# Performance work log

Hardware: AMD Instinct MI355X
Metric: run time of the kernel (lower is better)

The kernel has to match this reference:

```python
import jax, jax.numpy as jnp
import numpy as np

WS = 8          # window_size
SHIFT = 4       # shift_size
HEADS = 8
HD = 32         # head_dim
DIM = 256       # embedding_dim
PWS = 8         # pretrained_window_size
EPS = 1e-5


def _rel_tables():
    # log-spaced relative coords table, shape ((2*WS-1)^2, 2)
    r = np.arange(-(WS - 1), WS, dtype=np.float32)
    tb = np.stack(np.meshgrid(r, r, indexing='ij'), 0).reshape(2, -1).T
    tb = tb / (PWS - 1) * 8.0
    tb = np.sign(tb) * np.log2(np.abs(tb) + 1.0) / np.log2(8.0)
    # relative position index, shape (m, m)
    ch = np.arange(WS)
    coords = np.stack(np.meshgrid(ch, ch, indexing='ij'), 0).reshape(2, -1)
    rel = (coords[:, :, None] - coords[:, None, :]).transpose(1, 2, 0).astype(np.int64)
    rel[..., 0] += WS - 1
    rel[..., 1] += WS - 1
    rel[..., 0] *= 2 * WS - 1
    return tb.astype(np.float32), rel.sum(-1)


def _shift_mask(h, w):
    # standard Swin SW-MSA mask: region labels -> -100 where regions differ
    img = np.zeros((h, w), np.int32)
    cnt = 0
    for hs in (slice(0, h - WS), slice(h - WS, h - SHIFT), slice(h - SHIFT, h)):
        for wsl in (slice(0, w - WS), slice(w - WS, w - SHIFT), slice(w - SHIFT, w)):
            img[hs, wsl] = cnt
            cnt += 1
    nh, nw = h // WS, w // WS
    m = WS * WS
    mw = img.reshape(nh, WS, nw, WS).transpose(0, 2, 1, 3).reshape(nh * nw, m)
    return np.where(mw[:, None, :] != mw[:, :, None], -100.0, 0.0).astype(np.float32)


def _ln(x, g, b):
    mu = x.mean(-1, keepdims=True)
    var = ((x - mu) ** 2).mean(-1, keepdims=True)
    return (x - mu) * jax.lax.rsqrt(var + EPS) * g + b


def setup_inputs() -> dict:
    key = jax.random.key(0)
    ks = jax.random.split(key, 8)
    s = 0.02
    return {
        'x': jax.random.normal(ks[0], (2, DIM, 256, 256), jnp.float32),
        'qkv_w': jax.random.normal(ks[1], (DIM, 3 * HEADS * HD), jnp.float32) * s,
        'logit_scale': jnp.full((HEADS,), np.log(10.0), jnp.float32),
        'proj_w': jax.random.normal(ks[2], (HEADS * HD, DIM), jnp.float32) * s,
        'proj_b': jnp.zeros((DIM,), jnp.float32),
        'ln1_w': jnp.ones((DIM,), jnp.float32),
        'ln1_b': jnp.zeros((DIM,), jnp.float32),
        'fc1_w': jax.random.normal(ks[3], (DIM, 4 * DIM), jnp.float32) * s,
        'fc1_b': jnp.zeros((4 * DIM,), jnp.float32),
        'fc2_w': jax.random.normal(ks[4], (4 * DIM, DIM), jnp.float32) * s,
        'fc2_b': jnp.zeros((DIM,), jnp.float32),
        'ln2_w': jnp.ones((DIM,), jnp.float32),
        'ln2_b': jnp.zeros((DIM,), jnp.float32),
        'cpb_w1': jax.random.normal(ks[5], (2, 512), jnp.float32) * s,
        'cpb_b1': jnp.zeros((512,), jnp.float32),
        'cpb_w2': jax.random.normal(ks[6], (512, HEADS), jnp.float32) * s,
    }


def reference(x, qkv_w, logit_scale, proj_w, proj_b, ln1_w, ln1_b,
              fc1_w, fc1_b, fc2_w, fc2_b, ln2_w, ln2_b,
              cpb_w1, cpb_b1, cpb_w2):
    b, c, h, w = x.shape
    nh, nw = h // WS, w // WS
    Nw, m = nh * nw, WS * WS
    tb_np, idx_np = _rel_tables()
    smask = jnp.asarray(_shift_mask(h, w))              # (Nw, m, m)

    # cyclic shift
    xs = jnp.roll(x, (-SHIFT, -SHIFT), axis=(2, 3))

    # relative position bias via MLP, then 16*sigmoid
    bt = jax.nn.relu(jnp.asarray(tb_np) @ cpb_w1 + cpb_b1) @ cpb_w2   # (T, H)
    rpe = bt[jnp.asarray(idx_np).reshape(-1)].reshape(m, m, HEADS)
    bias = 16.0 * jax.nn.sigmoid(rpe.transpose(2, 0, 1))              # (H, m, m)
    amask = bias[None] + smask[:, None]                               # (Nw, H, m, m)

    # window partition: (b, c, h, w) -> (b, Nw, m, c)
    xw = xs.reshape(b, c, nh, WS, nw, WS).transpose(0, 2, 4, 3, 5, 1).reshape(b, Nw, m, c)

    # cosine attention
    qkv = (xw @ qkv_w).reshape(b, Nw, m, 3, HEADS, HD).transpose(3, 0, 1, 4, 2, 5)
    q, k, v = qkv[0], qkv[1], qkv[2]                                  # (b, Nw, H, m, HD)
    qn = q / jnp.maximum(jnp.linalg.norm(q, axis=-1, keepdims=True), 1e-12)
    kn = k / jnp.maximum(jnp.linalg.norm(k, axis=-1, keepdims=True), 1e-12)
    scale = jnp.exp(jnp.minimum(logit_scale, np.log(100.0)))          # (H,)
    logits = jnp.einsum('bnhid,bnhjd->bnhij', qn, kn) * scale[None, None, :, None, None]
    logits = logits + amask[None]
    p = jax.nn.softmax(logits, axis=-1)
    o = jnp.einsum('bnhij,bnhjd->bnhid', p, v)
    o = o.transpose(0, 1, 3, 2, 4).reshape(b, Nw, m, HEADS * HD) @ proj_w + proj_b

    # post-norm residuals
    y = _ln(o, ln1_w, ln1_b) + xw
    mlp = jax.nn.gelu(y @ fc1_w + fc1_b, approximate=False) @ fc2_w + fc2_b
    y = _ln(mlp, ln2_w, ln2_b) + y

    # window reverse + un-shift
    xr = y.reshape(b, nh, nw, WS, WS, c).transpose(0, 5, 1, 3, 2, 4).reshape(b, c, h, w)
    return jnp.roll(xr, (SHIFT, SHIFT), axis=(2, 3))
```

## Files before the change

### kernel.cpp

```cpp
#include <hip/hip_runtime.h>
#include <hip/hip_bf16.h>

typedef __attribute__((ext_vector_type(4))) float f32x4;
typedef __attribute__((ext_vector_type(8))) short s16x8;
typedef __attribute__((ext_vector_type(4))) unsigned short u16x4;

#define L_XW   0
#define L_SLAB 32768
#define L_NQ   131072
#define L_NK   133120
#define L_Y    131072
#define L_H0   0
#define L_H1   32768
#define L_H2   65536
#define L_H3   98304
#define L_MB   0
#define SMEM_BYTES 163840

#define WSO_BIAS   0
#define WSO_QKVW   131072
#define WSO_PROJW  524288
#define WSO_FC1W   655360
#define WSO_FC2W   1179648
#define WSO_SIN    1703936ULL
#define WSO_SOUT   68812800ULL

#define LOG2E 1.4426950408f

__device__ __forceinline__ unsigned short f2bf(float f) {
  __hip_bfloat16 h = __float2bfloat16(f);
  return __builtin_bit_cast(unsigned short, h);
}
__device__ __forceinline__ float bf2f(unsigned short b) {
  union { unsigned u; float f; } v; v.u = ((unsigned)b) << 16;
  return v.f;
}
__device__ __forceinline__ int swzb(int row, int byteoff) {
  return byteoff ^ ((row & 7) << 4);
}

__global__ __launch_bounds__(256)
void prep_kernel(const float* __restrict__ qkv_w,
                 const float* __restrict__ proj_w,
                 const float* __restrict__ fc1_w,
                 const float* __restrict__ fc2_w,
                 const float* __restrict__ cpb_w1,
                 const float* __restrict__ cpb_b1,
                 const float* __restrict__ cpb_w2,
                 const float* __restrict__ x,
                 const float* __restrict__ ls,
                 unsigned char* __restrict__ wsb) {
  __shared__ float tile[64][66];
  const int bid = blockIdx.x;
  const int tid = threadIdx.x;

  if (bid < 3072) {
    int e = bid * 256 + tid;
    const float* src; unsigned short* dst; int K, N; int eo; bool perm;
    if (e < 196608)       { eo = e;          src = qkv_w;  dst = (unsigned short*)(wsb + WSO_QKVW);  K = 256;  N = 768;  perm = false; }
    else if (e < 262144)  { eo = e - 196608; src = proj_w; dst = (unsigned short*)(wsb + WSO_PROJW); K = 256;  N = 256;  perm = true; }
    else if (e < 524288)  { eo = e - 262144; src = fc1_w;  dst = (unsigned short*)(wsb + WSO_FC1W);  K = 256;  N = 1024; perm = false; }
    else                  { eo = e - 524288; src = fc2_w;  dst = (unsigned short*)(wsb + WSO_FC2W);  K = 1024; N = 256;  perm = true; }
    int j = eo & 7, c = (eo >> 3) & 15, rest = eo >> 7;
    int Kg = K >> 3;
    int kg = rest % Kg, nt = rest / Kg;
    int s = kg * 8 + j;
    if (perm) s = (s & ~31) | ((s & 1) << 4) | ((s & 31) >> 1);
    dst[eo] = f2bf(src[s * N + nt * 16 + c]);
  } else if (bid == 3072) {
    float (*bt)[8] = (float(*)[8])&tile[0][0];
    for (int t = tid; t < 225; t += 256) {
      int a = t / 15, b = t % 15;
      float r0 = (float)(a - 7) * (8.0f / 7.0f);
      float r1 = (float)(b - 7) * (8.0f / 7.0f);
      float f0 = (r0 >= 0.f ? 1.f : -1.f) * log2f(fabsf(r0) + 1.f) * (1.f / 3.f);
      float f1 = (r1 >= 0.f ? 1.f : -1.f) * log2f(fabsf(r1) + 1.f) * (1.f / 3.f);
      float acc[8] = {0.f,0.f,0.f,0.f,0.f,0.f,0.f,0.f};
      for (int k = 0; k < 512; ++k) {
        float hv = f0 * cpb_w1[k] + f1 * cpb_w1[512 + k] + cpb_b1[k];
        hv = fmaxf(hv, 0.f);
        #pragma unroll
        for (int h = 0; h < 8; ++h) acc[h] += hv * cpb_w2[k * 8 + h];
      }
      #pragma unroll
      for (int h = 0; h < 8; ++h) bt[t][h] = acc[h];
    }
    __syncthreads();
    float* biasp = (float*)(wsb + WSO_BIAS);
    for (int e = tid; e < 32768; e += 256) {
      int nn = e & 3, cc = (e >> 2) & 15, i = (e >> 6) & 63, h = e >> 12;
      int j = nn * 16 + cc;
      int dr = (i >> 3) - (j >> 3) + 7, dc = (i & 7) - (j & 7) + 7;
      float v = bt[dr * 15 + dc][h];
      float scale = __expf(fminf(ls[h], 4.6051702f));
      biasp[e] = LOG2E * (16.f / (1.f + expf(-v)) - (scale + 16.f));
    }
  } else {
    int b2 = bid - 3073;
    int pb = b2 & 1023;
    int cg = (b2 >> 10) & 3;
    int b  = b2 >> 12;
    int p0 = pb * 64, c0 = cg * 64;
    unsigned short* sg = (unsigned short*)(wsb + WSO_SIN);

    int pi = tid & 63, cq = tid >> 6;
    for (int r = 0; r < 16; ++r) {
      int c = cq * 16 + r;
      tile[pi][c] = x[((size_t)(b * 256 + c0 + c)) * 65536 + p0 + pi];
    }
    __syncthreads();
    int po = tid >> 2, co = tid & 3;
    s16x8 pk0, pk1;
    #pragma unroll
    for (int j = 0; j < 8; ++j) {
      pk0[j] = (short)f2bf(tile[po][co * 16 + j]);
      pk1[j] = (short)f2bf(tile[po][co * 16 + 8 + j]);
    }
    unsigned short* dp = sg + ((size_t)b * 65536 + p0 + po) * 256 + c0 + co * 16;
    *(s16x8*)(dp) = pk0;
    *(s16x8*)(dp + 8) = pk1;
  }
}

__global__ __launch_bounds__(256)
void transpose_out_kernel(const unsigned char* __restrict__ wsb, float* __restrict__ out) {
  __shared__ float tile[64][65];
  int pb = blockIdx.x & 1023;
  int cg = (blockIdx.x >> 10) & 3;
  int b  = blockIdx.x >> 12;
  int p0 = pb * 64, c0 = cg * 64;
  int tid = threadIdx.x;
  const unsigned short* sg = (const unsigned short*)(wsb + WSO_SOUT);

  int pi = tid >> 2, cq = tid & 3;
  const unsigned short* rp = sg + ((size_t)b * 65536 + p0 + pi) * 256 + c0 + cq * 16;
  s16x8 a0 = *(const s16x8*)(rp);
  s16x8 a1 = *(const s16x8*)(rp + 8);
  #pragma unroll
  for (int j = 0; j < 8; ++j) {
    tile[pi][cq * 16 + j]     = bf2f((unsigned short)a0[j]);
    tile[pi][cq * 16 + 8 + j] = bf2f((unsigned short)a1[j]);
  }
  __syncthreads();
  int ci = tid >> 6, pi2 = tid & 63;
  for (int r = 0; r < 16; ++r) {
    int c = ci * 16 + r;
    out[((size_t)(b * 256 + c0 + c)) * 65536 + p0 + pi2] = tile[pi2][c];
  }
}

__global__ __launch_bounds__(512, 2)
void swin_block_kernel(const float* __restrict__ ls,
                       const float* __restrict__ proj_b,
                       const float* __restrict__ ln1w, const float* __restrict__ ln1b,
                       const float* __restrict__ fc1b,
                       const float* __restrict__ fc2b,
                       const float* __restrict__ ln2w, const float* __restrict__ ln2b,
                       unsigned char* __restrict__ wsb) {
  extern __shared__ char sm[];
  const int tid = threadIdx.x;
  const int w = tid >> 6;
  const int lane = tid & 63;
  const int g = lane >> 4;
  const int c16 = lane & 15;

  const int blk = blockIdx.x;
  const int bb = blk >> 10;
  const int widx = blk & 1023;
  const int wi = widx >> 5, wj = widx & 31;

  const f32x4* biasv = (const f32x4*)(wsb + WSO_BIAS);
  const unsigned short* qkvw = (const unsigned short*)(wsb + WSO_QKVW);
  const unsigned short* projw = (const unsigned short*)(wsb + WSO_PROJW);
  const unsigned short* fc1w = (const unsigned short*)(wsb + WSO_FC1W);
  const unsigned short* fc2w = (const unsigned short*)(wsb + WSO_FC2W);
  const unsigned short* sin_ = (const unsigned short*)(wsb + WSO_SIN);
  unsigned short* sout = (unsigned short*)(wsb + WSO_SOUT);

  #pragma unroll
  for (int it = 0; it < 4; ++it) {
    int u = tid + it * 512;
    int t = u >> 5, cu = u & 31;
    int rp = (wi * 8 + (t >> 3) + 4) & 255;
    int cp = (wj * 8 + (t & 7) + 4) & 255;
    size_t pix = (size_t)bb * 65536 + rp * 256 + cp;
    s16x8 v = *(const s16x8*)(sin_ + pix * 256 + cu * 8);
    *(s16x8*)(sm + L_XW + t * 512 + swzb(t, cu * 16)) = v;
  }
  __syncthreads();

  char* const QB = sm + L_SLAB + w * 12288;

  {
    int tiles[6] = {2*w, 2*w+1, 16+2*w, 17+2*w, 32+2*w, 33+2*w};
    f32x4 acc[6][4];
    #pragma unroll
    for (int a = 0; a < 6; ++a)
      #pragma unroll
      for (int b = 0; b < 4; ++b) acc[a][b] = f32x4{0.f,0.f,0.f,0.f};
    #pragma unroll 4
    for (int k0 = 0; k0 < 256; k0 += 32) {
      s16x8 af[4];
      #pragma unroll
      for (int mt = 0; mt < 4; ++mt) {
        int row = mt * 16 + c16;
        af[mt] = *(const s16x8*)(sm + L_XW + row * 512 + swzb(row, (k0 + g * 8) * 2));
      }
      #pragma unroll
      for (int ct = 0; ct < 6; ++ct) {
        s16x8 bfr = *(const s16x8*)(qkvw + ((tiles[ct] * 32 + (k0 >> 3) + g) * 16 + c16) * 8);
        #pragma unroll
        for (int mt = 0; mt < 4; ++mt)
          acc[ct][mt] = __builtin_amdgcn_mfma_f32_16x16x32_bf16(af[mt], bfr, acc[ct][mt], 0, 0, 0);
      }
    }
    #pragma unroll
    for (int mt = 0; mt < 4; ++mt)
      #pragma unroll
      for (int r = 0; r < 4; ++r) {
        int i = mt * 16 + 4 * g + r;
        unsigned uq = (unsigned)f2bf(acc[0][mt][r]) | ((unsigned)f2bf(acc[1][mt][r]) << 16);
        unsigned uk = (unsigned)f2bf(acc[2][mt][r]) | ((unsigned)f2bf(acc[3][mt][r]) << 16);
        *(unsigned*)(QB + i * 128 + swzb(i, c16 * 4)) = uq;
        *(unsigned*)(QB + i * 128 + swzb(i, 64 + c16 * 4)) = uk;
      }
    #pragma unroll
    for (int dt = 0; dt < 2; ++dt)
      #pragma unroll
      for (int r = 0; r < 4; ++r) {
        int d = dt * 16 + c16;
        u16x4 vv;
        #pragma unroll
        for (int mt = 0; mt < 4; ++mt) vv[mt] = f2bf(acc[4 + dt][mt][r]);
        *(u16x4*)(QB + 8192 + d * 128 + swzb(d, 8 * (4 * g + r))) = vv;
      }
  }
  {
    float lsc2 = LOG2E * __expf(fminf(ls[w], 4.6051702f));
    float sq = 0.f, sk2 = 0.f;
    #pragma unroll
    for (int cc4 = 0; cc4 < 4; ++cc4) {
      s16x8 qv = *(const s16x8*)(QB + lane * 128 + swzb(lane, cc4 * 16));
      s16x8 kv = *(const s16x8*)(QB + lane * 128 + swzb(lane, 64 + cc4 * 16));
      #pragma unroll
      for (int e = 0; e < 8; ++e) {
        float a = bf2f((unsigned short)qv[e]); sq  += a * a;
        float b = bf2f((unsigned short)kv[e]); sk2 += b * b;
      }
    }
    ((float*)(sm + L_NQ))[w * 64 + lane] = lsc2 * __builtin_amdgcn_rsqf(fmaxf(sq, 1e-24f));
    ((float*)(sm + L_NK))[w * 64 + lane] = __builtin_amdgcn_rsqf(fmaxf(sk2, 1e-24f));
  }

  {
    s16x8 qf[4];
    #pragma unroll
    for (int mt = 0; mt < 4; ++mt) {
      int row = mt * 16 + c16;
      qf[mt] = *(const s16x8*)(QB + row * 128 + swzb(row, g * 16));
    }
    f32x4 S[4][4];
    #pragma unroll
    for (int nt = 0; nt < 4; ++nt) {
      int row = nt * 16 + c16;
      s16x8 kf = *(const s16x8*)(QB + row * 128 + swzb(row, 64 + g * 16));
      #pragma unroll
      for (int mt = 0; mt < 4; ++mt)
        S[mt][nt] = __builtin_amdgcn_mfma_f32_16x16x32_bf16(qf[mt], kf, f32x4{0.f,0.f,0.f,0.f}, 0, 0, 0);
    }
    const float* nqp = (const float*)(sm + L_NQ) + w * 64;
    const float* nkp = (const float*)(sm + L_NK) + w * 64;
    float rk4[4];
    #pragma unroll
    for (int nt = 0; nt < 4; ++nt) rk4[nt] = nkp[nt * 16 + c16];

    const bool edge = (wi == 31) || (wj == 31);
    if (edge) {
      int labj[4];
      #pragma unroll
      for (int nt = 0; nt < 4; ++nt) {
        int jj = nt * 16 + c16;
        int tr = jj >> 3, tc = jj & 7;
        labj[nt] = ((wi == 31) ? (tr >= 4 ? 2 : 1) : 0) * 3 + ((wj == 31) ? (tc >= 4 ? 2 : 1) : 0);
      }
      #pragma unroll
      for (int mt = 0; mt < 4; ++mt)
        #pragma unroll
        for (int r = 0; r < 4; ++r) {
          int i = mt * 16 + 4 * g + r;
          float rq = nqp[i];
          f32x4 bb4 = biasv[(w * 64 + i) * 16 + c16];
          int tr = i >> 3, tc = i & 7;
          int labi = ((wi == 31) ? (tr >= 4 ? 2 : 1) : 0) * 3 + ((wj == 31) ? (tc >= 4 ? 2 : 1) : 0);
          u16x4 pk;
          #pragma unroll
          for (int nt = 0; nt < 4; ++nt) {
            float vx = fmaf(S[mt][nt][r] * rk4[nt], rq, bb4[nt]);
            if (labi != labj[nt]) vx -= 144.2695f;
            pk[nt] = f2bf(__builtin_amdgcn_exp2f(vx));
          }
          *(u16x4*)(QB + i * 128 + swzb(i, c16 * 8)) = pk;
        }
    } else {
      #pragma unroll
      for (int mt = 0; mt < 4; ++mt)
        #pragma unroll
        for (int r = 0; r < 4; ++r) {
          int i = mt * 16 + 4 * g + r;
          float rq = nqp[i];
          f32x4 bb4 = biasv[(w * 64 + i) * 16 + c16];
          u16x4 pk;
          #pragma unroll
          for (int nt = 0; nt < 4; ++nt) {
            float vx = fmaf(S[mt][nt][r] * rk4[nt], rq, bb4[nt]);
            pk[nt] = f2bf(__builtin_amdgcn_exp2f(vx));
          }
          *(u16x4*)(QB + i * 128 + swzb(i, c16 * 8)) = pk;
        }
    }

    s16x8 ones;
    #pragma unroll
    for (int e = 0; e < 8; ++e) ones[e] = (short)0x3F80;
    f32x4 O[4][2], RS[4];
    #pragma unroll
    for (int a = 0; a < 4; ++a) {
      O[a][0] = f32x4{0.f,0.f,0.f,0.f};
      O[a][1] = f32x4{0.f,0.f,0.f,0.f};
      RS[a]   = f32x4{0.f,0.f,0.f,0.f};
    }
    #pragma unroll
    for (int k0 = 0; k0 < 64; k0 += 32) {
      s16x8 pf[4];
      #pragma unroll
      for (int mt = 0; mt < 4; ++mt) {
        int row = mt * 16 + c16;
        pf[mt] = *(const s16x8*)(QB + row * 128 + swzb(row, (k0 + g * 8) * 2));
      }
      #pragma unroll
      for (int nt = 0; nt < 2; ++nt) {
        int d = nt * 16 + c16;
        s16x8 vf = *(const s16x8*)(QB + 8192 + d * 128 + swzb(d, (k0 + g * 8) * 2));
        #pragma unroll
        for (int mt = 0; mt < 4; ++mt)
          O[mt][nt] = __builtin_amdgcn_mfma_f32_16x16x32_bf16(pf[mt], vf, O[mt][nt], 0, 0, 0);
      }
      #pragma unroll
      for (int mt = 0; mt < 4; ++mt)
        RS[mt] = __builtin_amdgcn_mfma_f32_16x16x32_bf16(pf[mt], ones, RS[mt], 0, 0, 0);
    }
    #pragma unroll
    for (int mt = 0; mt < 4; ++mt)
      #pragma unroll
      for (int r = 0; r < 4; ++r) {
        float inv = __builtin_amdgcn_rcpf(fmaxf(RS[mt][r], 1e-35f));
        int i = mt * 16 + 4 * g + r;
        unsigned u = (unsigned)f2bf(O[mt][0][r] * inv) | ((unsigned)f2bf(O[mt][1][r] * inv) << 16);
        *(unsigned*)(QB + i * 128 + swzb(i, c16 * 4)) = u;
      }
  }
  __syncthreads();

  {
    f32x4 aP[2][4];
    #pragma unroll
    for (int a = 0; a < 2; ++a)
      #pragma unroll
      for (int b = 0; b < 4; ++b) aP[a][b] = f32x4{0.f,0.f,0.f,0.f};
    #pragma unroll 2
    for (int k0 = 0; k0 < 256; k0 += 32) {
      int hk = k0 >> 5;
      const char* OBk = sm + L_SLAB + hk * 12288;
      s16x8 af[4];
      #pragma unroll
      for (int mt = 0; mt < 4; ++mt) {
        int row = mt * 16 + c16;
        af[mt] = *(const s16x8*)(OBk + row * 128 + swzb(row, g * 16));
      }
      #pragma unroll
      for (int t2 = 0; t2 < 2; ++t2) {
        s16x8 bfr = *(const s16x8*)(projw + (((2*w + t2) * 32 + 4*hk + g) * 16 + c16) * 8);
        #pragma unroll
        for (int mt = 0; mt < 4; ++mt)
          aP[t2][mt] = __builtin_amdgcn_mfma_f32_16x16x32_bf16(af[mt], bfr, aP[t2][mt], 0, 0, 0);
      }
    }
    #pragma unroll
    for (int t2 = 0; t2 < 2; ++t2) {
      int col = (2*w + t2) * 16 + c16;
      float pb = proj_b[col];
      #pragma unroll
      for (int mt = 0; mt < 4; ++mt)
        #pragma unroll
        for (int r = 0; r < 4; ++r) {
          int i = mt * 16 + 4 * g + r;
          *(unsigned short*)(sm + L_Y + i * 512 + swzb(i, col * 2)) = f2bf(aP[t2][mt][r] + pb);
        }
    }
  }
  __syncthreads();

  {
    int t = tid >> 3, oc = tid & 7;
    float v[32];
    float s1 = 0.f;
    #pragma unroll
    for (int b2 = 0; b2 < 4; ++b2) {
      s16x8 vb = *(const s16x8*)(sm + L_Y + t * 512 + swzb(t, oc * 64 + b2 * 16));
      #pragma unroll
      for (int e = 0; e < 8; ++e) { float fv = bf2f((unsigned short)vb[e]); v[b2*8+e] = fv; s1 += fv; }
    }
    s1 += __shfl_xor(s1, 1);
    s1 += __shfl_xor(s1, 2);
    s1 += __shfl_xor(s1, 4);
    float mu = s1 * (1.f / 256.f);
    float s2 = 0.f;
    #pragma unroll
    for (int e = 0; e < 32; ++e) { float d = v[e] - mu; s2 += d * d; }
    s2 += __shfl_xor(s2, 1);
    s2 += __shfl_xor(s2, 2);
    s2 += __shfl_xor(s2, 4);
    float rs = __builtin_amdgcn_rsqf(s2 * (1.f / 256.f) + 1e-5f);
    #pragma unroll
    for (int b2 = 0; b2 < 4; ++b2) {
      s16x8 xb = *(const s16x8*)(sm + L_XW + t * 512 + swzb(t, oc * 64 + b2 * 16));
      s16x8 yb;
      #pragma unroll
      for (int e = 0; e < 8; ++e) {
        int c = oc * 32 + b2 * 8 + e;
        float yv = (v[b2*8+e] - mu) * rs * ln1w[c] + ln1b[c] + bf2f((unsigned short)xb[e]);
        yb[e] = (short)f2bf(yv);
      }
      *(s16x8*)(sm + L_Y + t * 512 + swzb(t, oc * 64 + b2 * 16)) = yb;
    }
  }
  __syncthreads();

  {
    const int Hoff[4] = {L_H0, L_H1, L_H2, L_H3};
    #pragma unroll 1
    for (int cp = 0; cp < 2; ++cp) {
      f32x4 acc1[2][2][4];
      #pragma unroll
      for (int a = 0; a < 2; ++a)
        #pragma unroll
        for (int b = 0; b < 2; ++b)
          #pragma unroll
          for (int m = 0; m < 4; ++m) acc1[a][b][m] = f32x4{0.f,0.f,0.f,0.f};
      for (int k0 = 0; k0 < 256; k0 += 32) {
        s16x8 af[4];
        #pragma unroll
        for (int mt = 0; mt < 4; ++mt) {
          int row = mt * 16 + c16;
          af[mt] = *(const s16x8*)(sm + L_Y + row * 512 + swzb(row, (k0 + g * 8) * 2));
        }
        #pragma unroll
        for (int cc2 = 0; cc2 < 2; ++cc2) {
          int cc = cp * 2 + cc2;
          #pragma unroll
          for (int t2 = 0; t2 < 2; ++t2) {
            int gt = cc * 16 + 2*w + t2;
            s16x8 bfr = *(const s16x8*)(fc1w + ((gt * 32 + (k0 >> 3) + g) * 16 + c16) * 8);
            #pragma unroll
            for (int mt = 0; mt < 4; ++mt)
              acc1[cc2][t2][mt] = __builtin_amdgcn_mfma_f32_16x16x32_bf16(af[mt], bfr, acc1[cc2][t2][mt], 0, 0, 0);
          }
        }
      }
      #pragma unroll
      for (int cc2 = 0; cc2 < 2; ++cc2) {
        int cc = cp * 2 + cc2;
        char* HB = sm + Hoff[cc];
        float b1v0 = fc1b[cc * 256 + 32 * w + c16];
        float b1v1 = fc1b[cc * 256 + 32 * w + 16 + c16];
        #pragma unroll
        for (int mt = 0; mt < 4; ++mt)
          #pragma unroll
          for (int r = 0; r < 4; ++r) {
            int i = mt * 16 + 4 * g + r;
            float u0 = acc1[cc2][0][mt][r] + b1v0;
            float u1 = acc1[cc2][1][mt][r] + b1v1;
            float e0 = __builtin_amdgcn_exp2f(-2.45538f * u0);
            float e1 = __builtin_amdgcn_exp2f(-2.45538f * u1);
            float g0 = u0 * __builtin_amdgcn_rcpf(1.f + e0);
            float g1 = u1 * __builtin_amdgcn_rcpf(1.f + e1);
            unsigned u = (unsigned)f2bf(g0) | ((unsigned)f2bf(g1) << 16);
            *(unsigned*)(HB + i * 512 + swzb(i, w * 64 + c16 * 4)) = u;
          }
      }
    }
  }
  __syncthreads();

  f32x4 acc2[2][4];
  #pragma unroll
  for (int a = 0; a < 2; ++a)
    #pragma unroll
    for (int b = 0; b < 4; ++b) acc2[a][b] = f32x4{0.f,0.f,0.f,0.f};
  {
    const int Hoff[4] = {L_H0, L_H1, L_H2, L_H3};
    #pragma unroll 1
    for (int cc = 0; cc < 4; ++cc) {
      const char* HB = sm + Hoff[cc];
      for (int k0 = 0; k0 < 256; k0 += 32) {
        s16x8 af[4];
        #pragma unroll
        for (int mt = 0; mt < 4; ++mt) {
          int row = mt * 16 + c16;
          af[mt] = *(const s16x8*)(HB + row * 512 + swzb(row, (k0 + g * 8) * 2));
        }
        #pragma unroll
        for (int t2 = 0; t2 < 2; ++t2) {
          int kg = cc * 32 + (k0 >> 3) + g;
          s16x8 bfr = *(const s16x8*)(fc2w + (((2*w + t2) * 128 + kg) * 16 + c16) * 8);
          #pragma unroll
          for (int mt = 0; mt < 4; ++mt)
            acc2[t2][mt] = __builtin_amdgcn_mfma_f32_16x16x32_bf16(af[mt], bfr, acc2[t2][mt], 0, 0, 0);
        }
      }
    }
  }
  __syncthreads();

  #pragma unroll
  for (int t2 = 0; t2 < 2; ++t2) {
    int col = (2*w + t2) * 16 + c16;
    float b2v = fc2b[col];
    #pragma unroll
    for (int mt = 0; mt < 4; ++mt)
      #pragma unroll
      for (int r = 0; r < 4; ++r) {
        int i = mt * 16 + 4 * g + r;
        *(unsigned short*)(sm + L_MB + i * 512 + swzb(i, col * 2)) = f2bf(acc2[t2][mt][r] + b2v);
      }
  }
  __syncthreads();

  {
    int t2 = tid >> 3, oc = tid & 7;
    float v[32];
    float s1 = 0.f;
    #pragma unroll
    for (int b2 = 0; b2 < 4; ++b2) {
      s16x8 vb = *(const s16x8*)(sm + L_MB + t2 * 512 + swzb(t2, oc * 64 + b2 * 16));
      #pragma unroll
      for (int e = 0; e < 8; ++e) { float fv = bf2f((unsigned short)vb[e]); v[b2*8+e] = fv; s1 += fv; }
    }
    s1 += __shfl_xor(s1, 1);
    s1 += __shfl_xor(s1, 2);
    s1 += __shfl_xor(s1, 4);
    float mu = s1 * (1.f / 256.f);
    float s2 = 0.f;
    #pragma unroll
    for (int e = 0; e < 32; ++e) { float d = v[e] - mu; s2 += d * d; }
    s2 += __shfl_xor(s2, 1);
    s2 += __shfl_xor(s2, 2);
    s2 += __shfl_xor(s2, 4);
    float rs = __builtin_amdgcn_rsqf(s2 * (1.f / 256.f) + 1e-5f);
    int rp = (wi * 8 + (t2 >> 3) + 4) & 255;
    int cp = (wj * 8 + (t2 & 7) + 4) & 255;
    size_t pix = (size_t)bb * 65536 + rp * 256 + cp;
    unsigned short* so = sout + pix * 256 + oc * 32;
    #pragma unroll
    for (int b2 = 0; b2 < 4; ++b2) {
      s16x8 yb = *(const s16x8*)(sm + L_Y + t2 * 512 + swzb(t2, oc * 64 + b2 * 16));
      s16x8 pk;
      #pragma unroll
      for (int e = 0; e < 8; ++e) {
        int c = oc * 32 + b2 * 8 + e;
        float yv = (v[b2*8+e] - mu) * rs * ln2w[c] + ln2b[c] + bf2f((unsigned short)yb[e]);
        pk[e] = (short)f2bf(yv);
      }
      *(s16x8*)(so + b2 * 8) = pk;
    }
  }
}

extern "C" void kernel_launch(void* const* d_in, const int* in_sizes, int n_in,
                              void* d_out, int out_size, void* d_ws, size_t ws_size,
                              hipStream_t stream) {
  const float* x      = (const float*)d_in[0];
  const float* qkv_w  = (const float*)d_in[1];
  const float* ls     = (const float*)d_in[2];
  const float* proj_w = (const float*)d_in[3];
  const float* proj_b = (const float*)d_in[4];
  const float* ln1w   = (const float*)d_in[5];
  const float* ln1b   = (const float*)d_in[6];
  const float* fc1_w  = (const float*)d_in[7];
  const float* fc1b   = (const float*)d_in[8];
  const float* fc2_w  = (const float*)d_in[9];
  const float* fc2b   = (const float*)d_in[10];
  const float* ln2w   = (const float*)d_in[11];
  const float* ln2b   = (const float*)d_in[12];
  const float* cpb_w1 = (const float*)d_in[13];
  const float* cpb_b1 = (const float*)d_in[14];
  const float* cpb_w2 = (const float*)d_in[15];
  unsigned char* wsb = (unsigned char*)d_ws;
  float* out = (float*)d_out;

  hipFuncSetAttribute(reinterpret_cast<const void*>(swin_block_kernel),
                      hipFuncAttributeMaxDynamicSharedMemorySize, SMEM_BYTES);

  prep_kernel<<<11265, 256, 0, stream>>>(qkv_w, proj_w, fc1_w, fc2_w,
                                         cpb_w1, cpb_b1, cpb_w2, x, ls, wsb);
  swin_block_kernel<<<2048, 512, SMEM_BYTES, stream>>>(
      ls, proj_b, ln1w, ln1b, fc1b, fc2b, ln2w, ln2b, wsb);
  transpose_out_kernel<<<8192, 256, 0, stream>>>(wsb, out);
}
```

Before: 472.1 us.

## Double workgroup size to 16 waves, splitting each head and GEMM column range

The fused Swin block kernel now launches 1024 threads per window instead of 512. Each attention head is split across two waves, each handling half the query rows, and the proj, fc1 and fc2 GEMMs give each wave half as many output columns. LayerNorm passes use 16 threads per token. This adds extra block-wide barriers and needs the smaller per-wave register footprint to fit the tighter launch bounds. With 160KB of LDS per block, occupancy stays at one block per CU, so the gain has to come from more waves in flight rather than more blocks.

```diff
diff --git a/kernel.cpp b/kernel.cpp
--- a/kernel.cpp
+++ b/kernel.cpp
@@ -149,7 +149,7 @@
   }
 }
 
-__global__ __launch_bounds__(512, 2)
+__global__ __launch_bounds__(1024, 4)
 void swin_block_kernel(const float* __restrict__ ls,
                        const float* __restrict__ proj_b,
                        const float* __restrict__ ln1w, const float* __restrict__ ln1b,
@@ -163,6 +163,9 @@
   const int lane = tid & 63;
   const int g = lane >> 4;
   const int c16 = lane & 15;
+  const int h = w >> 1;
+  const int half = w & 1;
+  const int mt0 = half * 2;
 
   const int blk = blockIdx.x;
   const int bb = blk >> 10;
@@ -178,8 +181,8 @@
   unsigned short* sout = (unsigned short*)(wsb + WSO_SOUT);
 
   #pragma unroll
-  for (int it = 0; it < 4; ++it) {
-    int u = tid + it * 512;
+  for (int it = 0; it < 2; ++it) {
+    int u = tid + it * 1024;
     int t = u >> 5, cu = u & 31;
     int rp = (wi * 8 + (t >> 3) + 4) & 255;
     int cp = (wj * 8 + (t & 7) + 4) & 255;
@@ -189,38 +192,38 @@
   }
   __syncthreads();
 
-  char* const QB = sm + L_SLAB + w * 12288;
-
-  {
-    int tiles[6] = {2*w, 2*w+1, 16+2*w, 17+2*w, 32+2*w, 33+2*w};
-    f32x4 acc[6][4];
+  char* const QB = sm + L_SLAB + h * 12288;
+
+  {
+    int tiles[6] = {2*h, 2*h+1, 16+2*h, 17+2*h, 32+2*h, 33+2*h};
+    f32x4 acc[6][2];
     #pragma unroll
     for (int a = 0; a < 6; ++a)
       #pragma unroll
-      for (int b = 0; b < 4; ++b) acc[a][b] = f32x4{0.f,0.f,0.f,0.f};
+      for (int b = 0; b < 2; ++b) acc[a][b] = f32x4{0.f,0.f,0.f,0.f};
     #pragma unroll 4
     for (int k0 = 0; k0 < 256; k0 += 32) {
-      s16x8 af[4];
-      #pragma unroll
-      for (int mt = 0; mt < 4; ++mt) {
-        int row = mt * 16 + c16;
-        af[mt] = *(const s16x8*)(sm + L_XW + row * 512 + swzb(row, (k0 + g * 8) * 2));
+      s16x8 af[2];
+      #pragma unroll
+      for (int j = 0; j < 2; ++j) {
+        int row = (mt0 + j) * 16 + c16;
+        af[j] = *(const s16x8*)(sm + L_XW + row * 512 + swzb(row, (k0 + g * 8) * 2));
       }
       #pragma unroll
       for (int ct = 0; ct < 6; ++ct) {
         s16x8 bfr = *(const s16x8*)(qkvw + ((tiles[ct] * 32 + (k0 >> 3) + g) * 16 + c16) * 8);
         #pragma unroll
-        for (int mt = 0; mt < 4; ++mt)
-          acc[ct][mt] = __builtin_amdgcn_mfma_f32_16x16x32_bf16(af[mt], bfr, acc[ct][mt], 0, 0, 0);
-      }
-    }
-    #pragma unroll
-    for (int mt = 0; mt < 4; ++mt)
+        for (int j = 0; j < 2; ++j)
+          acc[ct][j] = __builtin_amdgcn_mfma_f32_16x16x32_bf16(af[j], bfr, acc[ct][j], 0, 0, 0);
+      }
+    }
+    #pragma unroll
+    for (int j = 0; j < 2; ++j)
       #pragma unroll
       for (int r = 0; r < 4; ++r) {
-        int i = mt * 16 + 4 * g + r;
-        unsigned uq = (unsigned)f2bf(acc[0][mt][r]) | ((unsigned)f2bf(acc[1][mt][r]) << 16);
-        unsigned uk = (unsigned)f2bf(acc[2][mt][r]) | ((unsigned)f2bf(acc[3][mt][r]) << 16);
+        int i = (mt0 + j) * 16 + 4 * g + r;
+        unsigned uq = (unsigned)f2bf(acc[0][j][r]) | ((unsigned)f2bf(acc[1][j][r]) << 16);
+        unsigned uk = (unsigned)f2bf(acc[2][j][r]) | ((unsigned)f2bf(acc[3][j][r]) << 16);
         *(unsigned*)(QB + i * 128 + swzb(i, c16 * 4)) = uq;
         *(unsigned*)(QB + i * 128 + swzb(i, 64 + c16 * 4)) = uk;
       }
@@ -229,51 +232,52 @@
       #pragma unroll
       for (int r = 0; r < 4; ++r) {
         int d = dt * 16 + c16;
-        u16x4 vv;
-        #pragma unroll
-        for (int mt = 0; mt < 4; ++mt) vv[mt] = f2bf(acc[4 + dt][mt][r]);
-        *(u16x4*)(QB + 8192 + d * 128 + swzb(d, 8 * (4 * g + r))) = vv;
-      }
-  }
-  {
-    float lsc2 = LOG2E * __expf(fminf(ls[w], 4.6051702f));
+        unsigned uv = (unsigned)f2bf(acc[4 + dt][0][r]) | ((unsigned)f2bf(acc[4 + dt][1][r]) << 16);
+        *(unsigned*)(QB + 8192 + d * 128 + swzb(d, 8 * (4 * g + r) + 4 * half)) = uv;
+      }
+  }
+  if (lane < 32) {
+    int row = half * 32 + lane;
+    float lsc2 = LOG2E * __expf(fminf(ls[h], 4.6051702f));
     float sq = 0.f, sk2 = 0.f;
     #pragma unroll
     for (int cc4 = 0; cc4 < 4; ++cc4) {
-      s16x8 qv = *(const s16x8*)(QB + lane * 128 + swzb(lane, cc4 * 16));
-      s16x8 kv = *(const s16x8*)(QB + lane * 128 + swzb(lane, 64 + cc4 * 16));
+      s16x8 qv = *(const s16x8*)(QB + row * 128 + swzb(row, cc4 * 16));
+      s16x8 kv = *(const s16x8*)(QB + row * 128 + swzb(row, 64 + cc4 * 16));
       #pragma unroll
       for (int e = 0; e < 8; ++e) {
         float a = bf2f((unsigned short)qv[e]); sq  += a * a;
         float b = bf2f((unsigned short)kv[e]); sk2 += b * b;
       }
     }
-    ((float*)(sm + L_NQ))[w * 64 + lane] = lsc2 * __builtin_amdgcn_rsqf(fmaxf(sq, 1e-24f));
-    ((float*)(sm + L_NK))[w * 64 + lane] = __builtin_amdgcn_rsqf(fmaxf(sk2, 1e-24f));
-  }
-
-  {
-    s16x8 qf[4];
-    #pragma unroll
-    for (int mt = 0; mt < 4; ++mt) {
-      int row = mt * 16 + c16;
-      qf[mt] = *(const s16x8*)(QB + row * 128 + swzb(row, g * 16));
-    }
-    f32x4 S[4][4];
+    ((float*)(sm + L_NQ))[h * 64 + row] = lsc2 * __builtin_amdgcn_rsqf(fmaxf(sq, 1e-24f));
+    ((float*)(sm + L_NK))[h * 64 + row] = __builtin_amdgcn_rsqf(fmaxf(sk2, 1e-24f));
+  }
+  __syncthreads();
+
+  {
+    s16x8 qf[2];
+    #pragma unroll
+    for (int j = 0; j < 2; ++j) {
+      int row = (mt0 + j) * 16 + c16;
+      qf[j] = *(const s16x8*)(QB + row * 128 + swzb(row, g * 16));
+    }
+    f32x4 S[2][4];
     #pragma unroll
     for (int nt = 0; nt < 4; ++nt) {
       int row = nt * 16 + c16;
       s16x8 kf = *(const s16x8*)(QB + row * 128 + swzb(row, 64 + g * 16));
       #pragma unroll
-      for (int mt = 0; mt < 4; ++mt)
-        S[mt][nt] = __builtin_amdgcn_mfma_f32_16x16x32_bf16(qf[mt], kf, f32x4{0.f,0.f,0.f,0.f}, 0, 0, 0);
-    }
-    const float* nqp = (const float*)(sm + L_NQ) + w * 64;
-    const float* nkp = (const float*)(sm + L_NK) + w * 64;
+      for (int j = 0; j < 2; ++j)
+        S[j][nt] = __builtin_amdgcn_mfma_f32_16x16x32_bf16(qf[j], kf, f32x4{0.f,0.f,0.f,0.f}, 0, 0, 0);
+    }
+    const float* nqp = (const float*)(sm + L_NQ) + h * 64;
+    const float* nkp = (const float*)(sm + L_NK) + h * 64;
     float rk4[4];
     #pragma unroll
     for (int nt = 0; nt < 4; ++nt) rk4[nt] = nkp[nt * 16 + c16];
 
+    u16x4 pkv[2][4];
     const bool edge = (wi == 31) || (wj == 31);
     if (edge) {
       int labj[4];
@@ -284,92 +288,94 @@
         labj[nt] = ((wi == 31) ? (tr >= 4 ? 2 : 1) : 0) * 3 + ((wj == 31) ? (tc >= 4 ? 2 : 1) : 0);
       }
       #pragma unroll
-      for (int mt = 0; mt < 4; ++mt)
+      for (int j = 0; j < 2; ++j)
         #pragma unroll
         for (int r = 0; r < 4; ++r) {
-          int i = mt * 16 + 4 * g + r;
+          int i = (mt0 + j) * 16 + 4 * g + r;
           float rq = nqp[i];
-          f32x4 bb4 = biasv[(w * 64 + i) * 16 + c16];
+          f32x4 bb4 = biasv[(h * 64 + i) * 16 + c16];
           int tr = i >> 3, tc = i & 7;
           int labi = ((wi == 31) ? (tr >= 4 ? 2 : 1) : 0) * 3 + ((wj == 31) ? (tc >= 4 ? 2 : 1) : 0);
-          u16x4 pk;
           #pragma unroll
           for (int nt = 0; nt < 4; ++nt) {
-            float vx = fmaf(S[mt][nt][r] * rk4[nt], rq, bb4[nt]);
+            float vx = fmaf(S[j][nt][r] * rk4[nt], rq, bb4[nt]);
             if (labi != labj[nt]) vx -= 144.2695f;
-            pk[nt] = f2bf(__builtin_amdgcn_exp2f(vx));
+            pkv[j][r][nt] = f2bf(__builtin_amdgcn_exp2f(vx));
           }
-          *(u16x4*)(QB + i * 128 + swzb(i, c16 * 8)) = pk;
         }
     } else {
       #pragma unroll
-      for (int mt = 0; mt < 4; ++mt)
+      for (int j = 0; j < 2; ++j)
         #pragma unroll
         for (int r = 0; r < 4; ++r) {
-          int i = mt * 16 + 4 * g + r;
+          int i = (mt0 + j) * 16 + 4 * g + r;
           float rq = nqp[i];
-          f32x4 bb4 = biasv[(w * 64 + i) * 16 + c16];
-          u16x4 pk;
+          f32x4 bb4 = biasv[(h * 64 + i) * 16 + c16];
           #pragma unroll
           for (int nt = 0; nt < 4; ++nt) {
-            float vx = fmaf(S[mt][nt][r] * rk4[nt], rq, bb4[nt]);
-            pk[nt] = f2bf(__builtin_amdgcn_exp2f(vx));
+            float vx = fmaf(S[j][nt][r] * rk4[nt], rq, bb4[nt]);
+            pkv[j][r][nt] = f2bf(__builtin_amdgcn_exp2f(vx));
           }
-          *(u16x4*)(QB + i * 128 + swzb(i, c16 * 8)) = pk;
         }
     }
+    __syncthreads();
+
+    #pragma unroll
+    for (int j = 0; j < 2; ++j)
+      #pragma unroll
+      for (int r = 0; r < 4; ++r) {
+        int i = (mt0 + j) * 16 + 4 * g + r;
+        *(u16x4*)(QB + i * 128 + swzb(i, c16 * 8)) = pkv[j][r];
+      }
 
     s16x8 ones;
     #pragma unroll
     for (int e = 0; e < 8; ++e) ones[e] = (short)0x3F80;
-    f32x4 O[4][2], RS[4];
-    #pragma unroll
-    for (int a = 0; a < 4; ++a) {
+    f32x4 O[2][2], RS[2];
+    #pragma unroll
+    for (int a = 0; a < 2; ++a) {
       O[a][0] = f32x4{0.f,0.f,0.f,0.f};
       O[a][1] = f32x4{0.f,0.f,0.f,0.f};
       RS[a]   = f32x4{0.f,0.f,0.f,0.f};
     }
     #pragma unroll
     for (int k0 = 0; k0 < 64; k0 += 32) {
-      s16x8 pf[4];
-      #pragma unroll
-      for (int mt = 0; mt < 4; ++mt) {
-        int row = mt * 16 + c16;
-        pf[mt] = *(const s16x8*)(QB + row * 128 + swzb(row, (k0 + g * 8) * 2));
+      s16x8 pf[2];
+      #pragma unroll
+      for (int j = 0; j < 2; ++j) {
+        int row = (mt0 + j) * 16 + c16;
+        pf[j] = *(const s16x8*)(QB + row * 128 + swzb(row, (k0 + g * 8) * 2));
       }
       #pragma unroll
       for (int nt = 0; nt < 2; ++nt) {
         int d = nt * 16 + c16;
         s16x8 vf = *(const s16x8*)(QB + 8192 + d * 128 + swzb(d, (k0 + g * 8) * 2));
         #pragma unroll
-        for (int mt = 0; mt < 4; ++mt)
-          O[mt][nt] = __builtin_amdgcn_mfma_f32_16x16x32_bf16(pf[mt], vf, O[mt][nt], 0, 0, 0);
-      }
-      #pragma unroll
-      for (int mt = 0; mt < 4; ++mt)
-        RS[mt] = __builtin_amdgcn_mfma_f32_16x16x32_bf16(pf[mt], ones, RS[mt], 0, 0, 0);
-    }
-    #pragma unroll
-    for (int mt = 0; mt < 4; ++mt)
+        for (int j = 0; j < 2; ++j)
+          O[j][nt] = __builtin_amdgcn_mfma_f32_16x16x32_bf16(pf[j], vf, O[j][nt], 0, 0, 0);
+      }
+      #pragma unroll
+      for (int j = 0; j < 2; ++j)
+        RS[j] = __builtin_amdgcn_mfma_f32_16x16x32_bf16(pf[j], ones, RS[j], 0, 0, 0);
+    }
+    #pragma unroll
+    for (int j = 0; j < 2; ++j)
       #pragma unroll
       for (int r = 0; r < 4; ++r) {
-        float inv = __builtin_amdgcn_rcpf(fmaxf(RS[mt][r], 1e-35f));
-        int i = mt * 16 + 4 * g + r;
-        unsigned u = (unsigned)f2bf(O[mt][0][r] * inv) | ((unsigned)f2bf(O[mt][1][r] * inv) << 16);
+        float inv = __builtin_amdgcn_rcpf(fmaxf(RS[j][r], 1e-35f));
+        int i = (mt0 + j) * 16 + 4 * g + r;
+        unsigned u = (unsigned)f2bf(O[j][0][r] * inv) | ((unsigned)f2bf(O[j][1][r] * inv) << 16);
         *(unsigned*)(QB + i * 128 + swzb(i, c16 * 4)) = u;
       }
   }
   __syncthreads();
 
   {
-    f32x4 aP[2][4];
-    #pragma unroll
-    for (int a = 0; a < 2; ++a)
-      #pragma unroll
-      for (int b = 0; b < 4; ++b) aP[a][b] = f32x4{0.f,0.f,0.f,0.f};
+    f32x4 aP[4];
+    #pragma unroll
+    for (int b = 0; b < 4; ++b) aP[b] = f32x4{0.f,0.f,0.f,0.f};
     #pragma unroll 2
-    for (int k0 = 0; k0 < 256; k0 += 32) {
-      int hk = k0 >> 5;
+    for (int hk = 0; hk < 8; ++hk) {
       const char* OBk = sm + L_SLAB + hk * 12288;
       s16x8 af[4];
       #pragma unroll
@@ -377,126 +383,112 @@
         int row = mt * 16 + c16;
         af[mt] = *(const s16x8*)(OBk + row * 128 + swzb(row, g * 16));
       }
-      #pragma unroll
-      for (int t2 = 0; t2 < 2; ++t2) {
-        s16x8 bfr = *(const s16x8*)(projw + (((2*w + t2) * 32 + 4*hk + g) * 16 + c16) * 8);
-        #pragma unroll
-        for (int mt = 0; mt < 4; ++mt)
-          aP[t2][mt] = __builtin_amdgcn_mfma_f32_16x16x32_bf16(af[mt], bfr, aP[t2][mt], 0, 0, 0);
-      }
-    }
-    #pragma unroll
-    for (int t2 = 0; t2 < 2; ++t2) {
-      int col = (2*w + t2) * 16 + c16;
-      float pb = proj_b[col];
+      s16x8 bfr = *(const s16x8*)(projw + ((w * 32 + 4*hk + g) * 16 + c16) * 8);
       #pragma unroll
       for (int mt = 0; mt < 4; ++mt)
-        #pragma unroll
-        for (int r = 0; r < 4; ++r) {
-          int i = mt * 16 + 4 * g + r;
-          *(unsigned short*)(sm + L_Y + i * 512 + swzb(i, col * 2)) = f2bf(aP[t2][mt][r] + pb);
-        }
-    }
-  }
-  __syncthreads();
-
-  {
-    int t = tid >> 3, oc = tid & 7;
-    float v[32];
+        aP[mt] = __builtin_amdgcn_mfma_f32_16x16x32_bf16(af[mt], bfr, aP[mt], 0, 0, 0);
+    }
+    int col = w * 16 + c16;
+    float pb = proj_b[col];
+    #pragma unroll
+    for (int mt = 0; mt < 4; ++mt)
+      #pragma unroll
+      for (int r = 0; r < 4; ++r) {
+        int i = mt * 16 + 4 * g + r;
+        *(unsigned short*)(sm + L_Y + i * 512 + swzb(i, col * 2)) = f2bf(aP[mt][r] + pb);
+      }
+  }
+  __syncthreads();
+
+  {
+    int t = tid >> 4, lc = tid & 15;
+    float v[16];
     float s1 = 0.f;
     #pragma unroll
-    for (int b2 = 0; b2 < 4; ++b2) {
-      s16x8 vb = *(const s16x8*)(sm + L_Y + t * 512 + swzb(t, oc * 64 + b2 * 16));
+    for (int b2 = 0; b2 < 2; ++b2) {
+      s16x8 vb = *(const s16x8*)(sm + L_Y + t * 512 + swzb(t, lc * 32 + b2 * 16));
       #pragma unroll
       for (int e = 0; e < 8; ++e) { float fv = bf2f((unsigned short)vb[e]); v[b2*8+e] = fv; s1 += fv; }
     }
     s1 += __shfl_xor(s1, 1);
     s1 += __shfl_xor(s1, 2);
     s1 += __shfl_xor(s1, 4);
+    s1 += __shfl_xor(s1, 8);
     float mu = s1 * (1.f / 256.f);
     float s2 = 0.f;
     #pragma unroll
-    for (int e = 0; e < 32; ++e) { float d = v[e] - mu; s2 += d * d; }
+    for (int e = 0; e < 16; ++e) { float d = v[e] - mu; s2 += d * d; }
     s2 += __shfl_xor(s2, 1);
     s2 += __shfl_xor(s2, 2);
     s2 += __shfl_xor(s2, 4);
+    s2 += __shfl_xor(s2, 8);
     float rs = __builtin_amdgcn_rsqf(s2 * (1.f / 256.f) + 1e-5f);
     #pragma unroll
-    for (int b2 = 0; b2 < 4; ++b2) {
-      s16x8 xb = *(const s16x8*)(sm + L_XW + t * 512 + swzb(t, oc * 64 + b2 * 16));
+    for (int b2 = 0; b2 < 2; ++b2) {
+      s16x8 xb = *(const s16x8*)(sm + L_XW + t * 512 + swzb(t, lc * 32 + b2 * 16));
       s16x8 yb;
       #pragma unroll
       for (int e = 0; e < 8; ++e) {
-        int c = oc * 32 + b2 * 8 + e;
+        int c = lc * 16 + b2 * 8 + e;
         float yv = (v[b2*8+e] - mu) * rs * ln1w[c] + ln1b[c] + bf2f((unsigned short)xb[e]);
         yb[e] = (short)f2bf(yv);
       }
-      *(s16x8*)(sm + L_Y + t * 512 + swzb(t, oc * 64 + b2 * 16)) = yb;
+      *(s16x8*)(sm + L_Y + t * 512 + swzb(t, lc * 32 + b2 * 16)) = yb;
     }
   }
   __syncthreads();
 
   {
     const int Hoff[4] = {L_H0, L_H1, L_H2, L_H3};
-    #pragma unroll 1
-    for (int cp = 0; cp < 2; ++cp) {
-      f32x4 acc1[2][2][4];
-      #pragma unroll
-      for (int a = 0; a < 2; ++a)
-        #pragma unroll
-        for (int b = 0; b < 2; ++b)
-          #pragma unroll
-          for (int m = 0; m < 4; ++m) acc1[a][b][m] = f32x4{0.f,0.f,0.f,0.f};
-      for (int k0 = 0; k0 < 256; k0 += 32) {
-        s16x8 af[4];
-        #pragma unroll
-        for (int mt = 0; mt < 4; ++mt) {
-          int row = mt * 16 + c16;
-          af[mt] = *(const s16x8*)(sm + L_Y + row * 512 + swzb(row, (k0 + g * 8) * 2));
+    const int cc = w >> 2;
+    const int gt0 = cc * 16 + (w & 3) * 4;
+    char* HB = sm + Hoff[cc];
+    f32x4 acc1[4][4];
+    #pragma unroll
+    for (int a = 0; a < 4; ++a)
+      #pragma unroll
+      for (int m = 0; m < 4; ++m) acc1[a][m] = f32x4{0.f,0.f,0.f,0.f};
+    for (int k0 = 0; k0 < 256; k0 += 32) {
+      s16x8 af[4];
+      #pragma unroll
+      for (int mt = 0; mt < 4; ++mt) {
+        int row = mt * 16 + c16;
+        af[mt] = *(const s16x8*)(sm + L_Y + row * 512 + swzb(row, (k0 + g * 8) * 2));
+      }
+      #pragma unroll
+      for (int ct = 0; ct < 4; ++ct) {
+        s16x8 bfr = *(const s16x8*)(fc1w + (((gt0 + ct) * 32 + (k0 >> 3) + g) * 16 + c16) * 8);
+        #pragma unroll
+        for (int mt = 0; mt < 4; ++mt)
+          acc1[ct][mt] = __builtin_amdgcn_mfma_f32_16x16x32_bf16(af[mt], bfr, acc1[ct][mt], 0, 0, 0);
+      }
+    }
+    float b1v[4];
+    #pragma unroll
+    for (int ct = 0; ct < 4; ++ct) b1v[ct] = fc1b[(gt0 + ct) * 16 + c16];
+    #pragma unroll
+    for (int cp2 = 0; cp2 < 2; ++cp2) {
+      #pragma unroll
+      for (int mt = 0; mt < 4; ++mt)
+        #pragma unroll
+        for (int r = 0; r < 4; ++r) {
+          int i = mt * 16 + 4 * g + r;
+          float u0 = acc1[cp2 * 2][mt][r] + b1v[cp2 * 2];
+          float u1 = acc1[cp2 * 2 + 1][mt][r] + b1v[cp2 * 2 + 1];
+          float e0 = __builtin_amdgcn_exp2f(-2.45538f * u0);
+          float e1 = __builtin_amdgcn_exp2f(-2.45538f * u1);
+          float g0 = u0 * __builtin_amdgcn_rcpf(1.f + e0);
+          float g1 = u1 * __builtin_amdgcn_rcpf(1.f + e1);
+          unsigned u = (unsigned)f2bf(g0) | ((unsigned)f2bf(g1) << 16);
+          *(unsigned*)(HB + i * 512 + swzb(i, ((w & 3) * 2 + cp2) * 64 + c16 * 4)) = u;
         }
-        #pragma unroll
-        for (int cc2 = 0; cc2 < 2; ++cc2) {
-          int cc = cp * 2 + cc2;
-          #pragma unroll
-          for (int t2 = 0; t2 < 2; ++t2) {
-            int gt = cc * 16 + 2*w + t2;
-            s16x8 bfr = *(const s16x8*)(fc1w + ((gt * 32 + (k0 >> 3) + g) * 16 + c16) * 8);
-            #pragma unroll
-            for (int mt = 0; mt < 4; ++mt)
-              acc1[cc2][t2][mt] = __builtin_amdgcn_mfma_f32_16x16x32_bf16(af[mt], bfr, acc1[cc2][t2][mt], 0, 0, 0);
-          }
-        }
-      }
-      #pragma unroll
-      for (int cc2 = 0; cc2 < 2; ++cc2) {
-        int cc = cp * 2 + cc2;
-        char* HB = sm + Hoff[cc];
-        float b1v0 = fc1b[cc * 256 + 32 * w + c16];
-        float b1v1 = fc1b[cc * 256 + 32 * w + 16 + c16];
-        #pragma unroll
-        for (int mt = 0; mt < 4; ++mt)
-          #pragma unroll
-          for (int r = 0; r < 4; ++r) {
-            int i = mt * 16 + 4 * g + r;
-            float u0 = acc1[cc2][0][mt][r] + b1v0;
-            float u1 = acc1[cc2][1][mt][r] + b1v1;
-            float e0 = __builtin_amdgcn_exp2f(-2.45538f * u0);
-            float e1 = __builtin_amdgcn_exp2f(-2.45538f * u1);
-            float g0 = u0 * __builtin_amdgcn_rcpf(1.f + e0);
-            float g1 = u1 * __builtin_amdgcn_rcpf(1.f + e1);
-            unsigned u = (unsigned)f2bf(g0) | ((unsigned)f2bf(g1) << 16);
-            *(unsigned*)(HB + i * 512 + swzb(i, w * 64 + c16 * 4)) = u;
-          }
-      }
-    }
-  }
-  __syncthreads();
-
-  f32x4 acc2[2][4];
+    }
+  }
+  __syncthreads();
+
+  f32x4 acc2[4];
   #pragma unroll
-  for (int a = 0; a < 2; ++a)
-    #pragma unroll
-    for (int b = 0; b < 4; ++b) acc2[a][b] = f32x4{0.f,0.f,0.f,0.f};
+  for (int b = 0; b < 4; ++b) acc2[b] = f32x4{0.f,0.f,0.f,0.f};
   {
     const int Hoff[4] = {L_H0, L_H1, L_H2, L_H3};
     #pragma unroll 1
@@ -509,65 +501,63 @@
           int row = mt * 16 + c16;
           af[mt] = *(const s16x8*)(HB + row * 512 + swzb(row, (k0 + g * 8) * 2));
         }
-        #pragma unroll
-        for (int t2 = 0; t2 < 2; ++t2) {
-          int kg = cc * 32 + (k0 >> 3) + g;
-          s16x8 bfr = *(const s16x8*)(fc2w + (((2*w + t2) * 128 + kg) * 16 + c16) * 8);
-          #pragma unroll
-          for (int mt = 0; mt < 4; ++mt)
-            acc2[t2][mt] = __builtin_amdgcn_mfma_f32_16x16x32_bf16(af[mt], bfr, acc2[t2][mt], 0, 0, 0);
-        }
-      }
-    }
-  }
-  __syncthreads();
-
-  #pragma unroll
-  for (int t2 = 0; t2 < 2; ++t2) {
-    int col = (2*w + t2) * 16 + c16;
+        int kg = cc * 32 + (k0 >> 3) + g;
+        s16x8 bfr = *(const s16x8*)(fc2w + ((w * 128 + kg) * 16 + c16) * 8);
+        #pragma unroll
+        for (int mt = 0; mt < 4; ++mt)
+          acc2[mt] = __builtin_amdgcn_mfma_f32_16x16x32_bf16(af[mt], bfr, acc2[mt], 0, 0, 0);
+      }
+    }
+  }
+  __syncthreads();
+
+  {
+    int col = w * 16 + c16;
     float b2v = fc2b[col];
     #pragma unroll
     for (int mt = 0; mt < 4; ++mt)
       #pragma unroll
       for (int r = 0; r < 4; ++r) {
         int i = mt * 16 + 4 * g + r;
-        *(unsigned short*)(sm + L_MB + i * 512 + swzb(i, col * 2)) = f2bf(acc2[t2][mt][r] + b2v);
-      }
-  }
-  __syncthreads();
-
-  {
-    int t2 = tid >> 3, oc = tid & 7;
-    float v[32];
+        *(unsigned short*)(sm + L_MB + i * 512 + swzb(i, col * 2)) = f2bf(acc2[mt][r] + b2v);
+      }
+  }
+  __syncthreads();
+
+  {
+    int t2 = tid >> 4, lc = tid & 15;
+    float v[16];
     float s1 = 0.f;
     #pragma unroll
-    for (int b2 = 0; b2 < 4; ++b2) {
-      s16x8 vb = *(const s16x8*)(sm + L_MB + t2 * 512 + swzb(t2, oc * 64 + b2 * 16));
+    for (int b2 = 0; b2 < 2; ++b2) {
+      s16x8 vb = *(const s16x8*)(sm + L_MB + t2 * 512 + swzb(t2, lc * 32 + b2 * 16));
       #pragma unroll
       for (int e = 0; e < 8; ++e) { float fv = bf2f((unsigned short)vb[e]); v[b2*8+e] = fv; s1 += fv; }
     }
     s1 += __shfl_xor(s1, 1);
     s1 += __shfl_xor(s1, 2);
     s1 += __shfl_xor(s1, 4);
+    s1 += __shfl_xor(s1, 8);
     float mu = s1 * (1.f / 256.f);
     float s2 = 0.f;
     #pragma unroll
-    for (int e = 0; e < 32; ++e) { float d = v[e] - mu; s2 += d * d; }
+    for (int e = 0; e < 16; ++e) { float d = v[e] - mu; s2 += d * d; }
     s2 += __shfl_xor(s2, 1);
     s2 += __shfl_xor(s2, 2);
     s2 += __shfl_xor(s2, 4);
+    s2 += __shfl_xor(s2, 8);
     float rs = __builtin_amdgcn_rsqf(s2 * (1.f / 256.f) + 1e-5f);
     int rp = (wi * 8 + (t2 >> 3) + 4) & 255;
     int cp = (wj * 8 + (t2 & 7) + 4) & 255;
     size_t pix = (size_t)bb * 65536 + rp * 256 + cp;
-    unsigned short* so = sout + pix * 256 + oc * 32;
-    #pragma unroll
-    for (int b2 = 0; b2 < 4; ++b2) {
-      s16x8 yb = *(const s16x8*)(sm + L_Y + t2 * 512 + swzb(t2, oc * 64 + b2 * 16));
+    unsigned short* so = sout + pix * 256 + lc * 16;
+    #pragma unroll
+    for (int b2 = 0; b2 < 2; ++b2) {
+      s16x8 yb = *(const s16x8*)(sm + L_Y + t2 * 512 + swzb(t2, lc * 32 + b2 * 16));
       s16x8 pk;
       #pragma unroll
       for (int e = 0; e < 8; ++e) {
-        int c = oc * 32 + b2 * 8 + e;
+        int c = lc * 16 + b2 * 8 + e;
         float yv = (v[b2*8+e] - mu) * rs * ln2w[c] + ln2b[c] + bf2f((unsigned short)yb[e]);
         pk[e] = (short)f2bf(yv);
       }
@@ -603,7 +593,7 @@
 
   prep_kernel<<<11265, 256, 0, stream>>>(qkv_w, proj_w, fc1_w, fc2_w,
                                          cpb_w1, cpb_b1, cpb_w2, x, ls, wsb);
-  swin_block_kernel<<<2048, 512, SMEM_BYTES, stream>>>(
+  swin_block_kernel<<<2048, 1024, SMEM_BYTES, stream>>>(
       ls, proj_b, ln1w, ln1b, fc1b, fc2b, ln2w, ln2b, wsb);
   transpose_out_kernel<<<8192, 256, 0, stream>>>(wsb, out);
 }
```

Result: slower. 585.0 us (+23.9%).
